# Kernel tuning notes

Hardware: AMD Instinct MI355X
Metric: run time of the kernel (lower is better)

Reference implementation:

```python
import jax, jax.numpy as jnp
import numpy as np

ALPHA = 0.2
NEG_BIG = -9e15

def setup_inputs() -> dict:
    key = jax.random.key(0)
    k1, k2, k3, k4 = jax.random.split(key, 4)
    B, N, F = 8, 2048, 256
    h = jax.random.normal(k1, (B, N, F), dtype=jnp.float32)
    adj = jax.random.randint(k2, (B, N, N), 0, 2, dtype=jnp.int32)
    W = jax.random.normal(k3, (F, F), dtype=jnp.float32) * (1.414 / jnp.sqrt(F))
    a = jax.random.normal(k4, (2 * F, 1), dtype=jnp.float32) * 0.1
    return {"h": h, "adj": adj, "W": W, "a": a}

def reference(h, adj, W, a):
    F_out = W.shape[1]
    Wh = jnp.einsum('bnf,fo->bno', h, W)            # [B,N,F]
    Wh1 = Wh @ a[:F_out]                             # [B,N,1]
    Wh2 = Wh @ a[F_out:]                             # [B,N,1]
    e = jax.nn.leaky_relu(Wh1 + jnp.swapaxes(Wh2, 1, 2), negative_slope=ALPHA)  # [B,N,N]
    scores = jnp.where(adj > 0, e, NEG_BIG)
    attention = jax.nn.softmax(scores, axis=-1)      # [B,N,N]
    h_prime = jnp.einsum('bnm,bmf->bnf', attention, Wh)
    out = h + jax.nn.elu(h_prime)                    # concat=True -> elu; residual add
    return (out, attention)
```

## Files before the change

### kernel.cpp

```cpp
#include <hip/hip_runtime.h>

#define NB 8
#define NN 2048
#define NF 256

typedef __attribute__((ext_vector_type(8))) short bf16x8;
typedef __attribute__((ext_vector_type(4))) float f32x4;

__device__ __forceinline__ unsigned short f2bf(float x) {
  union { float f; unsigned int i; } c; c.f = x;
  unsigned int r = c.i + 0x7FFFu + ((c.i >> 16) & 1u);
  return (unsigned short)(r >> 16);
}
__device__ __forceinline__ unsigned short f2bf_fast(float x) {
  union { float f; unsigned int i; } c; c.f = x;
  return (unsigned short)((c.i + 0x8000u) >> 16);
}
__device__ __forceinline__ bf16x8 cvt8(float4 c0, float4 c1) {
  union { bf16x8 v8; unsigned short us[8]; } cu;
  cu.us[0] = f2bf_fast(c0.x); cu.us[1] = f2bf_fast(c0.y);
  cu.us[2] = f2bf_fast(c0.z); cu.us[3] = f2bf_fast(c0.w);
  cu.us[4] = f2bf_fast(c1.x); cu.us[5] = f2bf_fast(c1.y);
  cu.us[6] = f2bf_fast(c1.z); cu.us[7] = f2bf_fast(c1.w);
  return cu.v8;
}

__global__ __launch_bounds__(256) void k_prep(
    const float* __restrict__ W, const float* __restrict__ a,
    unsigned short* __restrict__ WT, float* __restrict__ u, float* __restrict__ v) {
  int t = threadIdx.x;
  if (blockIdx.x < 256) {
    int k = blockIdx.x;
    WT[t * 256 + k] = f2bf(W[k * 256 + t]);
  } else {
    float su = 0.f, sv = 0.f;
    for (int o = 0; o < 256; ++o) {
      float w = W[t * 256 + o];
      su += w * a[o];
      sv += w * a[256 + o];
    }
    u[t] = su; v[t] = sv;
  }
}

__global__ __launch_bounds__(256) void k_wht(
    const float* __restrict__ h, const unsigned short* __restrict__ WTr,
    unsigned short* __restrict__ WhT) {
  int bx = blockIdx.x;
  int b = bx >> 6;
  int t = bx & 63;
  int fBlk = (t >> 4) * 64;
  int iBlk = (t & 15) * 128;
  int wave = threadIdx.x >> 6, lane = threadIdx.x & 63;
  int fW = fBlk + (wave >> 1) * 32;
  int iW = iBlk + (wave & 1) * 64;
  int l15 = lane & 15, q8 = (lane >> 4) * 8;
  const float* hB = h + (size_t)b * NN * NF;

  f32x4 acc[2][4];
#pragma unroll
  for (int mt = 0; mt < 2; ++mt)
#pragma unroll
    for (int nt = 0; nt < 4; ++nt)
      acc[mt][nt] = (f32x4){0.f, 0.f, 0.f, 0.f};

  for (int k0 = 0; k0 < NF; k0 += 32) {
    int kk = k0 + q8;
    bf16x8 af[2], bfr[4];
#pragma unroll
    for (int mt = 0; mt < 2; ++mt) {
      int f = fW + mt * 16 + l15;
      af[mt] = *(const bf16x8*)(WTr + f * 256 + kk);
    }
#pragma unroll
    for (int nt = 0; nt < 4; ++nt) {
      int i = iW + nt * 16 + l15;
      const float* p = hB + (size_t)i * NF + kk;
      bfr[nt] = cvt8(*(const float4*)p, *(const float4*)(p + 4));
    }
#pragma unroll
    for (int mt = 0; mt < 2; ++mt)
#pragma unroll
      for (int nt = 0; nt < 4; ++nt)
        acc[mt][nt] = __builtin_amdgcn_mfma_f32_16x16x32_bf16(af[mt], bfr[nt], acc[mt][nt], 0, 0, 0);
  }

  unsigned short* WhTb = WhT + (size_t)b * NF * NN;
  int q4 = (lane >> 4) * 4;
#pragma unroll
  for (int mt = 0; mt < 2; ++mt)
#pragma unroll
    for (int nt = 0; nt < 4; ++nt)
#pragma unroll
      for (int r = 0; r < 4; ++r) {
        int f = fW + mt * 16 + q4 + r;
        int i = iW + nt * 16 + l15;
        WhTb[(size_t)f * NN + i] = f2bf(acc[mt][nt][r]);
      }
}

__global__ __launch_bounds__(256) void k_proj(
    const float* __restrict__ h, const float* __restrict__ u,
    const float* __restrict__ v, float* __restrict__ Wh1, float* __restrict__ Wh2) {
  int row = blockIdx.x * 4 + (threadIdx.x >> 6);
  int lane = threadIdx.x & 63;
  float4 hv = *(const float4*)(h + (size_t)row * NF + lane * 4);
  const float* up = u + lane * 4;
  const float* vp = v + lane * 4;
  float su = hv.x * up[0] + hv.y * up[1] + hv.z * up[2] + hv.w * up[3];
  float sv = hv.x * vp[0] + hv.y * vp[1] + hv.z * vp[2] + hv.w * vp[3];
#pragma unroll
  for (int off = 32; off >= 1; off >>= 1) {
    su += __shfl_xor(su, off);
    sv += __shfl_xor(sv, off);
  }
  if (lane == 0) { Wh1[row] = su; Wh2[row] = sv; }
}

__global__ __launch_bounds__(512, 4) void k_fuse(
    const int* __restrict__ adj, const float* __restrict__ Wh1,
    const float* __restrict__ Wh2, const unsigned short* __restrict__ WhT,
    const float* __restrict__ h, float* __restrict__ att, float* __restrict__ out) {
  __shared__ unsigned short satt[16 * 2048];
  const float NEGBIG = -9.0e15f;
  int bx = blockIdx.x;
  int b = bx >> 7;
  int i0 = (bx & 127) * 16;
  int wave = threadIdx.x >> 6, lane = threadIdx.x & 63;
  const float* w2 = Wh2 + ((size_t)b << 11);

  int rowbase = b * NN + i0 + wave * 2;
#pragma unroll
  for (int rr = 0; rr < 2; ++rr) {
    const int* arow = adj + (size_t)(rowbase + rr) * NN;
    float w1 = Wh1[rowbase + rr];
    float x[32];
#pragma unroll
    for (int c = 0; c < 8; ++c) {
      int j = c * 256 + lane * 4;
      int4 av = *(const int4*)(arow + j);
      float4 pv = *(const float4*)(w2 + j);
      float t;
      t = w1 + pv.x; t = t >= 0.f ? t : 0.2f * t; x[c*4+0] = (av.x > 0) ? t : NEGBIG;
      t = w1 + pv.y; t = t >= 0.f ? t : 0.2f * t; x[c*4+1] = (av.y > 0) ? t : NEGBIG;
      t = w1 + pv.z; t = t >= 0.f ? t : 0.2f * t; x[c*4+2] = (av.z > 0) ? t : NEGBIG;
      t = w1 + pv.w; t = t >= 0.f ? t : 0.2f * t; x[c*4+3] = (av.w > 0) ? t : NEGBIG;
    }

    float m = x[0];
#pragma unroll
    for (int k = 1; k < 32; ++k) m = fmaxf(m, x[k]);
#pragma unroll
    for (int off = 32; off >= 1; off >>= 1) m = fmaxf(m, __shfl_xor(m, off));
    float sum = 0.f;
#pragma unroll
    for (int k = 0; k < 32; ++k) { x[k] = __expf(x[k] - m); sum += x[k]; }
#pragma unroll
    for (int off = 32; off >= 1; off >>= 1) sum += __shfl_xor(sum, off);
    float iv = 1.0f / sum;

    int row_local = wave * 2 + rr;
    int swz = row_local * 8;
    float* orow = att + (size_t)(rowbase + rr) * NN;
    unsigned short* srow = satt + row_local * 2048;
#pragma unroll
    for (int c = 0; c < 8; ++c) {
      int j = c * 256 + lane * 4;
      float a0 = x[c*4+0] * iv, a1 = x[c*4+1] * iv;
      float a2 = x[c*4+2] * iv, a3 = x[c*4+3] * iv;
      *(float4*)(orow + j) = make_float4(a0, a1, a2, a3);
      int e = ((j & ~7) ^ swz) + (j & 7);
      union { short4 v4; unsigned short us[4]; } pk;
      pk.us[0] = f2bf_fast(a0); pk.us[1] = f2bf_fast(a1);
      pk.us[2] = f2bf_fast(a2); pk.us[3] = f2bf_fast(a3);
      *(short4*)(srow + e) = pk.v4;
    }
  }

  __syncthreads();

  int fW = wave * 32;
  int l15 = lane & 15, q8 = (lane >> 4) * 8;
  const unsigned short* WTb = WhT + (size_t)b * NF * NN;
  const unsigned short* aRow = satt + l15 * 2048;
  int swzA = l15 * 8;

  f32x4 acc[2];
#pragma unroll
  for (int nt = 0; nt < 2; ++nt) acc[nt] = (f32x4){0.f, 0.f, 0.f, 0.f};

  for (int kk = 0; kk < NN; kk += 32) {
    bf16x8 afr = *(const bf16x8*)(aRow + (((kk + q8) ^ swzA)));
    bf16x8 bfr[2];
#pragma unroll
    for (int nt = 0; nt < 2; ++nt) {
      int f = fW + nt * 16 + l15;
      bfr[nt] = *(const bf16x8*)(WTb + (size_t)f * NN + kk + q8);
    }
#pragma unroll
    for (int nt = 0; nt < 2; ++nt)
      acc[nt] = __builtin_amdgcn_mfma_f32_16x16x32_bf16(afr, bfr[nt], acc[nt], 0, 0, 0);
  }

  int q4 = (lane >> 4) * 4;
#pragma unroll
  for (int nt = 0; nt < 2; ++nt)
#pragma unroll
    for (int r = 0; r < 4; ++r) {
      int i = i0 + q4 + r;
      int f = fW + nt * 16 + l15;
      size_t idx = ((size_t)(b * NN + i)) * NF + f;
      float hp = acc[nt][r];
      float el = hp > 0.f ? hp : expm1f(hp);
      out[idx] = h[idx] + el;
    }
}

extern "C" void kernel_launch(void* const* d_in, const int* in_sizes, int n_in,
                              void* d_out, int out_size, void* d_ws, size_t ws_size,
                              hipStream_t stream) {
  const float* h = nullptr; const int* adj = nullptr;
  const float* W = nullptr; const float* a = nullptr;
  for (int i = 0; i < n_in; ++i) {
    int s = in_sizes[i];
    if (s == NB * NN * NF) h = (const float*)d_in[i];
    else if (s == NB * NN * NN) adj = (const int*)d_in[i];
    else if (s == NF * NF) W = (const float*)d_in[i];
    else if (s == 2 * NF) a = (const float*)d_in[i];
  }

  float* out = (float*)d_out;
  float* att = out + (size_t)NB * NN * NF;

  char* ws = (char*)d_ws;
  unsigned short* WhT = (unsigned short*)ws;
  unsigned short* WTr = (unsigned short*)(ws + 8388608);
  float* u   = (float*)(ws + 8388608 + 131072);
  float* v   = u + 256;
  float* Wh1 = v + 256;
  float* Wh2 = Wh1 + NB * NN;

  k_prep<<<257, 256, 0, stream>>>(W, a, WTr, u, v);
  k_wht<<<512, 256, 0, stream>>>(h, WTr, WhT);
  k_proj<<<NB * NN / 4, 256, 0, stream>>>(h, u, v, Wh1, Wh2);
  k_fuse<<<NB * 128, 512, 0, stream>>>(adj, Wh1, Wh2, WhT, h, att, out);
}
```

Measured before the change: 401.5 us.

## Split fused softmax/PV kernel into separate softmax and PV kernels

```diff
diff --git a/kernel.cpp b/kernel.cpp
--- a/kernel.cpp
+++ b/kernel.cpp
@@ -117,68 +117,77 @@
   if (lane == 0) { Wh1[row] = su; Wh2[row] = sv; }
 }
 
-__global__ __launch_bounds__(512, 4) void k_fuse(
+__global__ __launch_bounds__(256) void k_soft(
     const int* __restrict__ adj, const float* __restrict__ Wh1,
-    const float* __restrict__ Wh2, const unsigned short* __restrict__ WhT,
-    const float* __restrict__ h, float* __restrict__ att, float* __restrict__ out) {
-  __shared__ unsigned short satt[16 * 2048];
+    const float* __restrict__ Wh2, float* __restrict__ att) {
   const float NEGBIG = -9.0e15f;
+  int row = blockIdx.x * 4 + (threadIdx.x >> 6);
+  int lane = threadIdx.x & 63;
+  int b = row >> 11;
+  const float* w2 = Wh2 + (b << 11);
+  const int* arow = adj + (size_t)row * NN;
+  float w1 = Wh1[row];
+
+  float x[32];
+#pragma unroll
+  for (int c = 0; c < 8; ++c) {
+    int j = c * 256 + lane * 4;
+    int4 av = *(const int4*)(arow + j);
+    float4 pv = *(const float4*)(w2 + j);
+    float t;
+    t = w1 + pv.x; t = t >= 0.f ? t : 0.2f * t; x[c*4+0] = (av.x > 0) ? t : NEGBIG;
+    t = w1 + pv.y; t = t >= 0.f ? t : 0.2f * t; x[c*4+1] = (av.y > 0) ? t : NEGBIG;
+    t = w1 + pv.z; t = t >= 0.f ? t : 0.2f * t; x[c*4+2] = (av.z > 0) ? t : NEGBIG;
+    t = w1 + pv.w; t = t >= 0.f ? t : 0.2f * t; x[c*4+3] = (av.w > 0) ? t : NEGBIG;
+  }
+
+  float m = x[0];
+#pragma unroll
+  for (int k = 1; k < 32; ++k) m = fmaxf(m, x[k]);
+#pragma unroll
+  for (int off = 32; off >= 1; off >>= 1) m = fmaxf(m, __shfl_xor(m, off));
+  float sum = 0.f;
+#pragma unroll
+  for (int k = 0; k < 32; ++k) { x[k] = __expf(x[k] - m); sum += x[k]; }
+#pragma unroll
+  for (int off = 32; off >= 1; off >>= 1) sum += __shfl_xor(sum, off);
+  float iv = 1.0f / sum;
+
+  float* orow = att + (size_t)row * NN;
+#pragma unroll
+  for (int c = 0; c < 8; ++c) {
+    int j = c * 256 + lane * 4;
+    *(float4*)(orow + j) = make_float4(x[c*4+0] * iv, x[c*4+1] * iv,
+                                       x[c*4+2] * iv, x[c*4+3] * iv);
+  }
+}
+
+__global__ __launch_bounds__(512, 4) void k_pv(
+    const float* __restrict__ attf, const unsigned short* __restrict__ WhT,
+    const float* __restrict__ h, float* __restrict__ out) {
+  __shared__ __align__(16) unsigned short satt[16 * 2048];
   int bx = blockIdx.x;
   int b = bx >> 7;
   int i0 = (bx & 127) * 16;
-  int wave = threadIdx.x >> 6, lane = threadIdx.x & 63;
-  const float* w2 = Wh2 + ((size_t)b << 11);
-
-  int rowbase = b * NN + i0 + wave * 2;
-#pragma unroll
-  for (int rr = 0; rr < 2; ++rr) {
-    const int* arow = adj + (size_t)(rowbase + rr) * NN;
-    float w1 = Wh1[rowbase + rr];
-    float x[32];
+  int tid = threadIdx.x;
+
+  {
+    int r = tid >> 5;
+    int m0 = (tid & 31) * 8;
+    const float* arow = attf + ((size_t)(b * NN + i0 + r)) * NN;
+    unsigned short* srow = satt + r * 2048;
+    int swz = r * 8;
 #pragma unroll
     for (int c = 0; c < 8; ++c) {
-      int j = c * 256 + lane * 4;
-      int4 av = *(const int4*)(arow + j);
-      float4 pv = *(const float4*)(w2 + j);
-      float t;
-      t = w1 + pv.x; t = t >= 0.f ? t : 0.2f * t; x[c*4+0] = (av.x > 0) ? t : NEGBIG;
-      t = w1 + pv.y; t = t >= 0.f ? t : 0.2f * t; x[c*4+1] = (av.y > 0) ? t : NEGBIG;
-      t = w1 + pv.z; t = t >= 0.f ? t : 0.2f * t; x[c*4+2] = (av.z > 0) ? t : NEGBIG;
-      t = w1 + pv.w; t = t >= 0.f ? t : 0.2f * t; x[c*4+3] = (av.w > 0) ? t : NEGBIG;
-    }
-
-    float m = x[0];
-#pragma unroll
-    for (int k = 1; k < 32; ++k) m = fmaxf(m, x[k]);
-#pragma unroll
-    for (int off = 32; off >= 1; off >>= 1) m = fmaxf(m, __shfl_xor(m, off));
-    float sum = 0.f;
-#pragma unroll
-    for (int k = 0; k < 32; ++k) { x[k] = __expf(x[k] - m); sum += x[k]; }
-#pragma unroll
-    for (int off = 32; off >= 1; off >>= 1) sum += __shfl_xor(sum, off);
-    float iv = 1.0f / sum;
-
-    int row_local = wave * 2 + rr;
-    int swz = row_local * 8;
-    float* orow = att + (size_t)(rowbase + rr) * NN;
-    unsigned short* srow = satt + row_local * 2048;
-#pragma unroll
-    for (int c = 0; c < 8; ++c) {
-      int j = c * 256 + lane * 4;
-      float a0 = x[c*4+0] * iv, a1 = x[c*4+1] * iv;
-      float a2 = x[c*4+2] * iv, a3 = x[c*4+3] * iv;
-      *(float4*)(orow + j) = make_float4(a0, a1, a2, a3);
-      int e = ((j & ~7) ^ swz) + (j & 7);
-      union { short4 v4; unsigned short us[4]; } pk;
-      pk.us[0] = f2bf_fast(a0); pk.us[1] = f2bf_fast(a1);
-      pk.us[2] = f2bf_fast(a2); pk.us[3] = f2bf_fast(a3);
-      *(short4*)(srow + e) = pk.v4;
-    }
-  }
-
+      int j = c * 256 + m0;
+      float4 p0 = *(const float4*)(arow + j);
+      float4 p1 = *(const float4*)(arow + j + 4);
+      *(bf16x8*)(srow + (j ^ swz)) = cvt8(p0, p1);
+    }
+  }
   __syncthreads();
 
+  int wave = tid >> 6, lane = tid & 63;
   int fW = wave * 32;
   int l15 = lane & 15, q8 = (lane >> 4) * 8;
   const unsigned short* WTb = WhT + (size_t)b * NF * NN;
@@ -243,5 +252,6 @@
   k_prep<<<257, 256, 0, stream>>>(W, a, WTr, u, v);
   k_wht<<<512, 256, 0, stream>>>(h, WTr, WhT);
   k_proj<<<NB * NN / 4, 256, 0, stream>>>(h, u, v, Wh1, Wh2);
-  k_fuse<<<NB * 128, 512, 0, stream>>>(adj, Wh1, Wh2, WhT, h, att, out);
-}
+  k_soft<<<NB * NN / 4, 256, 0, stream>>>(adj, Wh1, Wh2, att);
+  k_pv<<<NB * 128, 512, 0, stream>>>(att, WhT, h, out);
+}
```

After: 426.6 us. +6.3%, slower.

## Merge Wh GEMM and projection kernels, retile GEMM, remap fused-kernel block order

Applied to the files above, without the earlier changes.

```diff
diff --git a/kernel.cpp b/kernel.cpp
--- a/kernel.cpp
+++ b/kernel.cpp
@@ -43,78 +43,59 @@
   }
 }
 
-__global__ __launch_bounds__(256) void k_wht(
+__global__ __launch_bounds__(256) void k_mid(
     const float* __restrict__ h, const unsigned short* __restrict__ WTr,
-    unsigned short* __restrict__ WhT) {
+    const float* __restrict__ u, const float* __restrict__ v,
+    unsigned short* __restrict__ WhT, float* __restrict__ Wh1, float* __restrict__ Wh2) {
   int bx = blockIdx.x;
-  int b = bx >> 6;
-  int t = bx & 63;
-  int fBlk = (t >> 4) * 64;
-  int iBlk = (t & 15) * 128;
-  int wave = threadIdx.x >> 6, lane = threadIdx.x & 63;
-  int fW = fBlk + (wave >> 1) * 32;
-  int iW = iBlk + (wave & 1) * 64;
-  int l15 = lane & 15, q8 = (lane >> 4) * 8;
-  const float* hB = h + (size_t)b * NN * NF;
-
-  f32x4 acc[2][4];
-#pragma unroll
-  for (int mt = 0; mt < 2; ++mt)
-#pragma unroll
-    for (int nt = 0; nt < 4; ++nt)
-      acc[mt][nt] = (f32x4){0.f, 0.f, 0.f, 0.f};
-
-  for (int k0 = 0; k0 < NF; k0 += 32) {
-    int kk = k0 + q8;
-    bf16x8 af[2], bfr[4];
-#pragma unroll
-    for (int mt = 0; mt < 2; ++mt) {
-      int f = fW + mt * 16 + l15;
-      af[mt] = *(const bf16x8*)(WTr + f * 256 + kk);
-    }
-#pragma unroll
-    for (int nt = 0; nt < 4; ++nt) {
-      int i = iW + nt * 16 + l15;
-      const float* p = hB + (size_t)i * NF + kk;
-      bfr[nt] = cvt8(*(const float4*)p, *(const float4*)(p + 4));
-    }
-#pragma unroll
-    for (int mt = 0; mt < 2; ++mt)
-#pragma unroll
-      for (int nt = 0; nt < 4; ++nt)
-        acc[mt][nt] = __builtin_amdgcn_mfma_f32_16x16x32_bf16(af[mt], bfr[nt], acc[mt][nt], 0, 0, 0);
-  }
-
-  unsigned short* WhTb = WhT + (size_t)b * NF * NN;
-  int q4 = (lane >> 4) * 4;
-#pragma unroll
-  for (int mt = 0; mt < 2; ++mt)
-#pragma unroll
-    for (int nt = 0; nt < 4; ++nt)
+  if (bx < 256) {
+    int b = bx >> 5;
+    int i64 = (bx & 31) * 64;
+    int wave = threadIdx.x >> 6, lane = threadIdx.x & 63;
+    int iW = i64 + wave * 16;
+    int l15 = lane & 15, q8 = (lane >> 4) * 8;
+    const float* hB = h + (size_t)b * NN * NF;
+
+    f32x4 acc[16];
+#pragma unroll
+    for (int ft = 0; ft < 16; ++ft) acc[ft] = (f32x4){0.f, 0.f, 0.f, 0.f};
+
+    for (int k0 = 0; k0 < NF; k0 += 32) {
+      int kk = k0 + q8;
+      const float* p = hB + (size_t)(iW + l15) * NF + kk;
+      bf16x8 bfr = cvt8(*(const float4*)p, *(const float4*)(p + 4));
+#pragma unroll
+      for (int ft = 0; ft < 16; ++ft) {
+        bf16x8 af = *(const bf16x8*)(WTr + (ft * 16 + l15) * 256 + kk);
+        acc[ft] = __builtin_amdgcn_mfma_f32_16x16x32_bf16(af, bfr, acc[ft], 0, 0, 0);
+      }
+    }
+
+    unsigned short* WhTb = WhT + (size_t)b * NF * NN;
+    int q4 = (lane >> 4) * 4;
+#pragma unroll
+    for (int ft = 0; ft < 16; ++ft)
 #pragma unroll
       for (int r = 0; r < 4; ++r) {
-        int f = fW + mt * 16 + q4 + r;
-        int i = iW + nt * 16 + l15;
-        WhTb[(size_t)f * NN + i] = f2bf(acc[mt][nt][r]);
+        int f = ft * 16 + q4 + r;
+        int i = iW + l15;
+        WhTb[(size_t)f * NN + i] = f2bf(acc[ft][r]);
       }
-}
-
-__global__ __launch_bounds__(256) void k_proj(
-    const float* __restrict__ h, const float* __restrict__ u,
-    const float* __restrict__ v, float* __restrict__ Wh1, float* __restrict__ Wh2) {
-  int row = blockIdx.x * 4 + (threadIdx.x >> 6);
-  int lane = threadIdx.x & 63;
-  float4 hv = *(const float4*)(h + (size_t)row * NF + lane * 4);
-  const float* up = u + lane * 4;
-  const float* vp = v + lane * 4;
-  float su = hv.x * up[0] + hv.y * up[1] + hv.z * up[2] + hv.w * up[3];
-  float sv = hv.x * vp[0] + hv.y * vp[1] + hv.z * vp[2] + hv.w * vp[3];
-#pragma unroll
-  for (int off = 32; off >= 1; off >>= 1) {
-    su += __shfl_xor(su, off);
-    sv += __shfl_xor(sv, off);
-  }
-  if (lane == 0) { Wh1[row] = su; Wh2[row] = sv; }
+  } else {
+    int row = (bx - 256) * 4 + (threadIdx.x >> 6);
+    int lane = threadIdx.x & 63;
+    float4 hv = *(const float4*)(h + (size_t)row * NF + lane * 4);
+    const float* up = u + lane * 4;
+    const float* vp = v + lane * 4;
+    float su = hv.x * up[0] + hv.y * up[1] + hv.z * up[2] + hv.w * up[3];
+    float sv = hv.x * vp[0] + hv.y * vp[1] + hv.z * vp[2] + hv.w * vp[3];
+#pragma unroll
+    for (int off = 32; off >= 1; off >>= 1) {
+      su += __shfl_xor(su, off);
+      sv += __shfl_xor(sv, off);
+    }
+    if (lane == 0) { Wh1[row] = su; Wh2[row] = sv; }
+  }
 }
 
 __global__ __launch_bounds__(512, 4) void k_fuse(
@@ -124,6 +105,7 @@
   __shared__ unsigned short satt[16 * 2048];
   const float NEGBIG = -9.0e15f;
   int bx = blockIdx.x;
+  bx = (bx & 7) * 128 + (bx >> 3);
   int b = bx >> 7;
   int i0 = (bx & 127) * 16;
   int wave = threadIdx.x >> 6, lane = threadIdx.x & 63;
@@ -241,7 +223,6 @@
   float* Wh2 = Wh1 + NB * NN;
 
   k_prep<<<257, 256, 0, stream>>>(W, a, WTr, u, v);
-  k_wht<<<512, 256, 0, stream>>>(h, WTr, WhT);
-  k_proj<<<NB * NN / 4, 256, 0, stream>>>(h, u, v, Wh1, Wh2);
+  k_mid<<<256 + NB * NN / 4, 256, 0, stream>>>(h, WTr, u, v, WhT, Wh1, Wh2);
   k_fuse<<<NB * 128, 512, 0, stream>>>(adj, Wh1, Wh2, WhT, h, att, out);
 }
```

Result: slower. 412.9 us (+2.9%).
